# Performance work log

Hardware: AMD Instinct MI355X
Metric: run time of the kernel (lower is better)

The kernel has to match this reference:

```python
import jax, jax.numpy as jnp
import numpy as np

ITERATIONS = 50
EPS = 1.0        # entropy_epsilon
LAM = 1.0
TAU = 1.0 * EPS  # tau = 1 * entropy_epsilon
HALF = 2         # ker_halfsize
SIGMA = 5.0
DN = ('NCHW', 'OIHW', 'NCHW')


def _std_kernel():
    r = jnp.arange(-HALF, HALF + 1, dtype=jnp.float32)
    xx, yy = jnp.meshgrid(r, r, indexing='ij')
    k = jnp.exp(-(xx ** 2 + yy ** 2) / (2.0 * SIGMA ** 2))
    k = k / (k.sum() + 1e-15)
    return k[None, None]  # [1,1,5,5]


_NABLA = jnp.array([[[[0., 0., 0.], [0., -1., 0.], [0., 1., 0.]]],
                    [[[0., 0., 0.], [0., -1., 1.], [0., 0., 0.]]]], dtype=jnp.float32)  # [2,1,3,3]
_DIV = jnp.array([[[[0., -1., 0.], [0., 1., 0.], [0., 0., 0.]],
                   [[0., 0., 0.], [-1., 1., 0.], [0., 0., 0.]]]], dtype=jnp.float32)    # [1,2,3,3]


def _conv(x, w, pad):
    return jax.lax.conv_general_dilated(x, w, (1, 1), [(pad, pad), (pad, pad)],
                                        dimension_numbers=DN)


def setup_inputs() -> dict:
    key = jax.random.key(0)
    o = jax.random.normal(key, (8, 1, 512, 512), dtype=jnp.float32)
    return {"o": o}


def reference(o):
    o = o[:, 0]                      # squeeze channel dim -> [B,H,W]
    B, H, W = o.shape
    ker = _std_kernel()
    # torch.meshgrid(arange(1,H+1), arange(1,W+1)) with 'ij' indexing
    x = jnp.broadcast_to(jnp.arange(1, H + 1, dtype=jnp.float32)[:, None], (H, W))
    y = jnp.broadcast_to(jnp.arange(1, W + 1, dtype=jnp.float32)[None, :], (H, W))

    u0 = jax.nn.sigmoid(o / EPS)
    q0 = jnp.zeros_like(o)

    def step(carry, _):
        u, q, _p, _Tq = carry
        p = _conv(1.0 - 2.0 * u[:, None], ker, HALF)[:, 0]          # [B,H,W]
        s = u.sum((1, 2))                                           # [B]
        cx = (u * x).sum((1, 2)) / s
        cy = (u * y).sum((1, 2)) / s
        dx = x[None] - cx[:, None, None]                            # [B,H,W]
        dy = y[None] - cy[:, None, None]
        cossin = (dx * dy * u).sum((1, 2)) / s
        bsin = (dx ** 2 * u).sum((1, 2)) / s
        asin = (dy ** 2 * u).sum((1, 2)) / s
        Tx = -dx * cossin[:, None, None] + dy * bsin[:, None, None]
        Ty = dy * cossin[:, None, None] - dx * asin[:, None, None]
        Tn = jnp.sqrt(Tx ** 2 + Ty ** 2) + 1e-10
        Tx = Tx / Tn
        Ty = Ty / Tn
        un = _conv(u[:, None], _NABLA, 1)                           # [B,2,H,W]
        q_new = q - TAU * (un[:, 0] * Tx + un[:, 1] * Ty)
        Tq = _conv(jnp.stack([Tx * q_new, Ty * q_new], axis=1), _DIV, 1)[:, 0]
        u_new = jax.nn.sigmoid((o - LAM * p - Tq) / EPS)
        return (u_new, q_new, p, Tq), None

    (u, q, p, Tq), _ = jax.lax.scan(step, (u0, q0, q0, q0), None, length=ITERATIONS)
    u1 = (o - LAM * p - Tq) / EPS
    return u1
```

## Files before the change

### kernel.cpp

```cpp
#include <hip/hip_runtime.h>
#include <math.h>

typedef _Float16 h16;
typedef h16 half8v __attribute__((ext_vector_type(8)));
typedef h16 half4v __attribute__((ext_vector_type(4)));
typedef h16 half2v __attribute__((ext_vector_type(2)));

#define HH 512
#define WW 512
#define BB 8
#define NPIX (HH*WW)
#define NTOT (BB*NPIX)
#define ITER 50

#define TX 64
#define TILE_ROWS 64

#define BLK_PER_BATCH 64
#define PART_ITER_STRIDE (BB*BLK_PER_BATCH*8)

constexpr double W0d = 0.92311634638663587;
constexpr double W1d = 0.98019867330675525;
constexpr double SUM1D = 1.0 + 2.0*(W0d + W1d);
constexpr float  INV_NORM = (float)(1.0/(SUM1D*SUM1D + 1e-15));
constexpr float  W0f = (float)W0d;
constexpr float  W1f = (float)W1d;
constexpr float  S1f = (float)SUM1D;

__device__ __forceinline__ float fast_sigmoid(float x) {
    const float e = __expf(-x);
    return __builtin_amdgcn_rcpf(1.0f + e);
}

__device__ __forceinline__ float edge1d(int v) {
    float r = S1f;
    if (v == 0 || v == HH - 1) r = S1f - W0f - W1f;
    else if (v == 1 || v == HH - 2) r = S1f - W0f;
    return r;
}

union U32H2 { unsigned u; h16 h[2]; };

__device__ __forceinline__ void reduce6_store(float v[6], float* dst8) {
    #pragma unroll
    for (int kk = 0; kk < 6; kk++) {
        float x = v[kk];
        #pragma unroll
        for (int off = 32; off > 0; off >>= 1) x += __shfl_down(x, off, 64);
        v[kk] = x;
    }
    __shared__ float sm[4][6];
    const int lane = threadIdx.x & 63;
    const int wv   = threadIdx.x >> 6;
    if (lane == 0) {
        #pragma unroll
        for (int kk = 0; kk < 6; kk++) sm[wv][kk] = v[kk];
    }
    __syncthreads();
    if (threadIdx.x == 0) {
        float tt[6];
        #pragma unroll
        for (int kk = 0; kk < 6; kk++) tt[kk] = sm[0][kk] + sm[1][kk] + sm[2][kk] + sm[3][kk];
        *(float4*)dst8       = make_float4(tt[0], tt[1], tt[2], tt[3]);
        *(float4*)(dst8 + 4) = make_float4(tt[4], tt[5], 0.f, 0.f);
    }
}

__device__ __forceinline__ void evalF(float uc, float ud, float ur, float qv,
                                      float dx, float dy,
                                      float cossin, float bsin, float asin_,
                                      float& a, float& bv, float& qn) {
    float Tx = -dx * cossin + dy * bsin;
    float Ty =  dy * cossin - dx * asin_;
    const float rn = __builtin_amdgcn_rsqf(Tx * Tx + Ty * Ty + 1e-20f);
    Tx *= rn; Ty *= rn;
    qn = qv - ((ud - uc) * Tx + (ur - uc) * Ty);
    a  = Tx * qn;
    bv = Ty * qn;
}

__global__ __launch_bounds__(256) void init_kernel(const float* __restrict__ o,
                                                   h16* __restrict__ u,
                                                   h16* __restrict__ q,
                                                   h16* __restrict__ oh,
                                                   float* __restrict__ part0) {
    const int b     = blockIdx.x & 7;
    const int chunk = blockIdx.x >> 3;
    const int within = chunk * 4096 + threadIdx.x * 16;
    const int pix = b * NPIX + within;
    const int i = within >> 9;
    const int j = within & (WW - 1);

    float of[16];
    #pragma unroll
    for (int s = 0; s < 4; s++) {
        const float4 ov = *(const float4*)(o + pix + 4 * s);
        of[4*s+0] = ov.x; of[4*s+1] = ov.y; of[4*s+2] = ov.z; of[4*s+3] = ov.w;
    }

    half8v oh8[2], uh8[2], qz8[2];
    float urf[16];
    #pragma unroll
    for (int kk = 0; kk < 16; kk++) {
        oh8[kk >> 3][kk & 7] = (h16)of[kk];
        uh8[kk >> 3][kk & 7] = (h16)fast_sigmoid(of[kk]);
        urf[kk] = (float)uh8[kk >> 3][kk & 7];
        qz8[kk >> 3][kk & 7] = (h16)0.f;
    }
    *(half8v*)(u + pix)      = uh8[0];
    *(half8v*)(u + pix + 8)  = uh8[1];
    *(half8v*)(q + pix)      = qz8[0];
    *(half8v*)(q + pix + 8)  = qz8[1];
    *(half8v*)(oh + pix)     = oh8[0];
    *(half8v*)(oh + pix + 8) = oh8[1];

    const float x = (float)(i + 1);
    float s0 = 0.f, sy = 0.f, syy = 0.f;
    #pragma unroll
    for (int kk = 0; kk < 16; kk++) {
        const float y = (float)(j + 1 + kk);
        s0 += urf[kk]; sy += urf[kk] * y; syy += urf[kk] * y * y;
    }
    float v[6] = {s0, x * s0, sy, x * sy, x * x * s0, syy};
    reduce6_store(v, part0 + ((size_t)b * BLK_PER_BATCH + chunk) * 8);
}

__global__ __launch_bounds__(256) void step_kernel(const h16* __restrict__ oh,
                                                   const h16* __restrict__ uA,
                                                   const h16* __restrict__ qA,
                                                   h16* __restrict__ uB,
                                                   h16* __restrict__ qB,
                                                   const float* __restrict__ partIn,
                                                   float* __restrict__ partOut,
                                                   float* __restrict__ out,
                                                   int lastFlag) {
    const int b    = blockIdx.x & 7;
    const int tile = blockIdx.x >> 3;
    const int j0 = (tile & 7) * TX;
    const int i0 = (tile >> 3) * TILE_ROWS;
    const h16* ubase = uA + (size_t)b * NPIX;
    const h16* qbase = qA + (size_t)b * NPIX;

    const int lin  = threadIdx.x;
    const int lane = lin & 63;
    const int tx = lin & 7;
    const int ty = lin >> 3;
    const int ia = i0 + 2 * ty;
    const int jb = j0 + 8 * tx;
    const int loffA = ia * WW + jb;
    const int loffB = loffA + WW;
    const size_t goffA = (size_t)b * NPIX + loffA;
    const size_t goffB = goffA + WW;

    const bool lok = (jb > 0);
    const bool rok = (jb + 8 < WW);
    const bool ltx = (tx > 0);
    const bool rtx = (tx < 7);

    const float* P0 = partIn + (size_t)b * (BLK_PER_BATCH * 8) + lane * 8;
    const float4 pA0 = *(const float4*)P0;
    const float4 pB0 = *(const float4*)(P0 + 4);

    half8v uM[6];
    unsigned uLbw[6], uRbw[6];
    #pragma unroll
    for (int r = 0; r < 6; r++) {
        const int ii = ia - 2 + r;
        const bool rowok = (ii >= 0 && ii < HH);
        half8v m;
        #pragma unroll
        for (int c = 0; c < 8; c++) m[c] = (h16)0.f;
        unsigned lw = 0u, rw = 0u;
        if (rowok) {
            const h16* rowp = ubase + ii * WW;
            m = *(const half8v*)(rowp + jb);
            if (!ltx && lok) lw = *(const unsigned*)(rowp + jb - 2);
            if (!rtx && rok) rw = *(const unsigned*)(rowp + jb + 8);
        }
        uM[r] = m; uLbw[r] = lw; uRbw[r] = rw;
    }
    const half8v qcA8 = *(const half8v*)(qbase + loffA);
    const half8v qcB8 = *(const half8v*)(qbase + loffB);
    const half8v qu8  = *(const half8v*)(qbase + ((ia > 0) ? loffA - WW : loffA));
    h16 qlA_g = (h16)0.f, qlB_g = (h16)0.f;
    if (!ltx && lok) {
        qlA_g = qbase[loffA - 1];
        qlB_g = qbase[loffB - 1];
    }
    const half8v oA8  = *(const half8v*)(oh + goffA);
    const half8v oB8  = *(const half8v*)(oh + goffB);

    float v6[6] = {pA0.x, pA0.y, pA0.z, pA0.w, pB0.x, pB0.y};
    #pragma unroll
    for (int mask = 1; mask < 64; mask <<= 1) {
        #pragma unroll
        for (int c = 0; c < 6; c++) v6[c] += __shfl_xor(v6[c], mask, 64);
    }
    const double sS  = (double)v6[0];
    const double inv = 1.0 / sS;
    const double cxd = (double)v6[1] * inv;
    const double cyd = (double)v6[2] * inv;
    const float cxf    = (float)cxd;
    const float cyf    = (float)cyd;
    const float cossin = (float)((double)v6[3] * inv - cxd * cyd);
    const float bsin   = (float)((double)v6[4] * inv - cxd * cxd);
    const float asin_  = (float)((double)v6[5] * inv - cyd * cyd);

    unsigned uLw[6], uRw[6];
    #pragma unroll
    for (int r = 0; r < 6; r++) {
        const unsigned w3 = ((const unsigned*)&uM[r])[3];
        const unsigned w0 = ((const unsigned*)&uM[r])[0];
        const unsigned fromL = (unsigned)__shfl((int)w3, lane - 1, 64);
        const unsigned fromR = (unsigned)__shfl((int)w0, lane + 1, 64);
        uLw[r] = ltx ? fromL : uLbw[r];
        uRw[r] = rtx ? fromR : uRbw[r];
    }
    h16 qlAh, qlBh;
    {
        const unsigned qa3 = ((const unsigned*)&qcA8)[3];
        const unsigned qb3 = ((const unsigned*)&qcB8)[3];
        U32H2 ca, cb;
        ca.u = (unsigned)__shfl((int)qa3, lane - 1, 64);
        cb.u = (unsigned)__shfl((int)qb3, lane - 1, 64);
        qlAh = ltx ? ca.h[1] : qlA_g;
        qlBh = ltx ? cb.h[1] : qlB_g;
    }

    float vsA[12], vsB[12];
    float Ue[4][10];
    constexpr float wAr[6] = {W0f, W1f, 1.f, W1f, W0f, 0.f};
    constexpr float wBr[6] = {0.f, W0f, W1f, 1.f, W1f, W0f};
    #pragma unroll
    for (int r = 0; r < 6; r++) {
        float U[12];
        U32H2 cl, cr;
        cl.u = uLw[r]; cr.u = uRw[r];
        U[0] = (float)cl.h[0]; U[1] = (float)cl.h[1];
        #pragma unroll
        for (int c = 0; c < 8; c++) U[c + 2] = (float)uM[r][c];
        U[10] = (float)cr.h[0]; U[11] = (float)cr.h[1];
        #pragma unroll
        for (int c = 0; c < 12; c++) {
            if (r == 0)             vsA[c] = wAr[0] * U[c];
            else if (wAr[r] != 0.f) vsA[c] += wAr[r] * U[c];
            if (r == 1)             vsB[c] = wBr[1] * U[c];
            else if (wBr[r] != 0.f) vsB[c] += wBr[r] * U[c];
        }
        if (r >= 1 && r <= 4) {
            #pragma unroll
            for (int c = 0; c < 10; c++) Ue[r - 1][c] = U[c + 1];
        }
    }

    const float RiA = edge1d(ia);
    const float RiB = edge1d(ia + 1);
    const float dxA = (float)(ia + 1) - cxf;
    const float dxB = (float)(ia + 2) - cxf;
    const float dxu = (float)ia - cxf;

    float blA = 0.f, blB = 0.f;
    {
        const float dyl = (float)jb - cyf;
        float ad, bl, qd;
        evalF(Ue[1][0], Ue[2][0], Ue[1][1], (float)qlAh,
              dxA, dyl, cossin, bsin, asin_, ad, bl, qd);
        if (lok) blA = bl;
        evalF(Ue[2][0], Ue[3][0], Ue[2][1], (float)qlBh,
              dxB, dyl, cossin, bsin, asin_, ad, bl, qd);
        if (lok) blB = bl;
    }

    half8v uhA, uhB, qhA, qhB;
    float s0A = 0.f, syA = 0.f, syyA = 0.f, s0B = 0.f, syB = 0.f, syyB = 0.f;
    float bA_prev = blA, bB_prev = blB;
    #pragma unroll
    for (int k = 0; k < 8; k++) {
        const float Rj = edge1d(jb + k);
        const float cA = W0f * (vsA[k] + vsA[k + 4]) + W1f * (vsA[k + 1] + vsA[k + 3]) + vsA[k + 2];
        const float cB = W0f * (vsB[k] + vsB[k + 4]) + W1f * (vsB[k + 1] + vsB[k + 3]) + vsB[k + 2];
        const float p4A = INV_NORM * (RiA * Rj - 2.0f * cA);
        const float p4B = INV_NORM * (RiB * Rj - 2.0f * cB);

        const float dy = (float)(jb + k + 1) - cyf;
        float aA, bA, qnA;
        evalF(Ue[1][k + 1], Ue[2][k + 1], Ue[1][k + 2], (float)qcA8[k],
              dxA, dy, cossin, bsin, asin_, aA, bA, qnA);
        float au, bu_d, qu_d;
        evalF(Ue[0][k + 1], Ue[1][k + 1], Ue[0][k + 2], (float)qu8[k],
              dxu, dy, cossin, bsin, asin_, au, bu_d, qu_d);
        const float aUA = (ia > 0) ? au : 0.f;
        float aB, bB, qnB;
        evalF(Ue[2][k + 1], Ue[3][k + 1], Ue[2][k + 2], (float)qcB8[k],
              dxB, dy, cossin, bsin, asin_, aB, bB, qnB);

        const float TqA = aA + bA - aUA - bA_prev;
        const float TqB = aB + bB - aA - bB_prev;
        const float tAv = (float)oA8[k] - p4A - TqA;
        const float tBv = (float)oB8[k] - p4B - TqB;

        uhA[k] = (h16)fast_sigmoid(tAv);
        uhB[k] = (h16)fast_sigmoid(tBv);
        qhA[k] = (h16)qnA;
        qhB[k] = (h16)qnB;

        const float urA = (float)uhA[k];
        const float urB = (float)uhB[k];
        const float y = (float)(jb + k + 1);
        s0A += urA; syA += urA * y; syyA += urA * y * y;
        s0B += urB; syB += urB * y; syyB += urB * y * y;

        if (lastFlag) {
            out[goffA + k] = tAv;
            out[goffB + k] = tBv;
        }
        bA_prev = bA; bB_prev = bB;
    }

    *(half8v*)(uB + goffA) = uhA;
    *(half8v*)(uB + goffB) = uhB;
    *(half8v*)(qB + goffA) = qhA;
    *(half8v*)(qB + goffB) = qhB;
    if (lastFlag) return;

    const float xA = (float)(ia + 1);
    const float xB = (float)(ia + 2);
    float v[6] = {s0A + s0B, xA * s0A + xB * s0B, syA + syB,
                  xA * syA + xB * syB, xA * xA * s0A + xB * xB * s0B, syyA + syyB};
    reduce6_store(v, partOut + ((size_t)b * BLK_PER_BATCH + tile) * 8);
}

extern "C" void kernel_launch(void* const* d_in, const int* in_sizes, int n_in,
                              void* d_out, int out_size, void* d_ws, size_t ws_size,
                              hipStream_t stream) {
    const float* o = (const float*)d_in[0];
    float* out = (float*)d_out;

    h16* uA = (h16*)d_ws;
    h16* uB = uA + (size_t)NTOT;
    h16* qA = uB + (size_t)NTOT;
    h16* qB = qA + (size_t)NTOT;
    h16* oh = qB + (size_t)NTOT;
    float* partials = (float*)(oh + (size_t)NTOT);

    init_kernel<<<512, 256, 0, stream>>>(o, uA, qA, oh, partials);

    h16 *ua = uA, *ub = uB, *qa = qA, *qb = qB;
    for (int k = 0; k < ITER; k++) {
        step_kernel<<<512, 256, 0, stream>>>(
            oh, ua, qa, ub, qb,
            partials + (size_t)k * PART_ITER_STRIDE,
            partials + (size_t)(k + 1) * PART_ITER_STRIDE,
            out, (k == ITER - 1) ? 1 : 0);
        h16* tmp;
        tmp = ua; ua = ub; ub = tmp;
        tmp = qa; qa = qb; qb = tmp;
    }
}
```

Measured before the change: 517.4 us.

## Fuse iteration launches into one persistent kernel with per-batch flag barriers

```diff
diff --git a/kernel.cpp b/kernel.cpp
--- a/kernel.cpp
+++ b/kernel.cpp
@@ -3,8 +3,6 @@
 
 typedef _Float16 h16;
 typedef h16 half8v __attribute__((ext_vector_type(8)));
-typedef h16 half4v __attribute__((ext_vector_type(4)));
-typedef h16 half2v __attribute__((ext_vector_type(2)));
 
 #define HH 512
 #define WW 512
@@ -17,7 +15,8 @@
 #define TILE_ROWS 64
 
 #define BLK_PER_BATCH 64
-#define PART_ITER_STRIDE (BB*BLK_PER_BATCH*8)
+#define SLOTF 8
+#define PART_PAR_STRIDE (BB*BLK_PER_BATCH*SLOTF)
 
 constexpr double W0d = 0.92311634638663587;
 constexpr double W1d = 0.98019867330675525;
@@ -27,6 +26,22 @@
 constexpr float  W1f = (float)W1d;
 constexpr float  S1f = (float)SUM1D;
 
+__device__ __forceinline__ unsigned long long ald64(const void* p) {
+    return __hip_atomic_load((unsigned long long*)p, __ATOMIC_RELAXED, __HIP_MEMORY_SCOPE_AGENT);
+}
+__device__ __forceinline__ unsigned ald32(const void* p) {
+    return __hip_atomic_load((unsigned*)p, __ATOMIC_RELAXED, __HIP_MEMORY_SCOPE_AGENT);
+}
+__device__ __forceinline__ void ast64(void* p, unsigned long long v) {
+    __hip_atomic_store((unsigned long long*)p, v, __ATOMIC_RELAXED, __HIP_MEMORY_SCOPE_AGENT);
+}
+__device__ __forceinline__ void ast32(void* p, unsigned v) {
+    __hip_atomic_store((unsigned*)p, v, __ATOMIC_RELAXED, __HIP_MEMORY_SCOPE_AGENT);
+}
+union H8U  { half8v h; unsigned long long u[2]; unsigned w[4]; };
+union U32H2 { unsigned u; h16 h[2]; };
+union U64F2 { unsigned long long u; float f[2]; };
+
 __device__ __forceinline__ float fast_sigmoid(float x) {
     const float e = __expf(-x);
     return __builtin_amdgcn_rcpf(1.0f + e);
@@ -39,9 +54,7 @@
     return r;
 }
 
-union U32H2 { unsigned u; h16 h[2]; };
-
-__device__ __forceinline__ void reduce6_store(float v[6], float* dst8) {
+__device__ __forceinline__ void reduce6_store_tagged(float v[6], float* dst8, float tag) {
     #pragma unroll
     for (int kk = 0; kk < 6; kk++) {
         float x = v[kk];
@@ -61,8 +74,15 @@
         float tt[6];
         #pragma unroll
         for (int kk = 0; kk < 6; kk++) tt[kk] = sm[0][kk] + sm[1][kk] + sm[2][kk] + sm[3][kk];
-        *(float4*)dst8       = make_float4(tt[0], tt[1], tt[2], tt[3]);
-        *(float4*)(dst8 + 4) = make_float4(tt[4], tt[5], 0.f, 0.f);
+        U64F2 w0, w1, w2;
+        w0.f[0] = tt[0]; w0.f[1] = tt[1];
+        w1.f[0] = tt[2]; w1.f[1] = tt[3];
+        w2.f[0] = tt[4]; w2.f[1] = tt[5];
+        ast64(dst8,     w0.u);
+        ast64(dst8 + 2, w1.u);
+        ast64(dst8 + 4, w2.u);
+        asm volatile("s_waitcnt vmcnt(0)" ::: "memory");
+        ast32(dst8 + 7, __float_as_uint(tag));
     }
 }
 
@@ -83,13 +103,18 @@
                                                    h16* __restrict__ u,
                                                    h16* __restrict__ q,
                                                    h16* __restrict__ oh,
-                                                   float* __restrict__ part0) {
+                                                   float* __restrict__ parts) {
     const int b     = blockIdx.x & 7;
     const int chunk = blockIdx.x >> 3;
     const int within = chunk * 4096 + threadIdx.x * 16;
     const int pix = b * NPIX + within;
     const int i = within >> 9;
     const int j = within & (WW - 1);
+
+    if (threadIdx.x == 0) {
+        float* slot0 = parts + ((size_t)b * BLK_PER_BATCH + chunk) * SLOTF;
+        ast32(slot0 + 7, __float_as_uint(0.0f));
+    }
 
     float of[16];
     #pragma unroll
@@ -113,6 +138,7 @@
     *(half8v*)(q + pix + 8)  = qz8[1];
     *(half8v*)(oh + pix)     = oh8[0];
     *(half8v*)(oh + pix + 8) = oh8[1];
+    asm volatile("s_waitcnt vmcnt(0)" ::: "memory");
 
     const float x = (float)(i + 1);
     float s0 = 0.f, sy = 0.f, syy = 0.f;
@@ -122,24 +148,22 @@
         s0 += urf[kk]; sy += urf[kk] * y; syy += urf[kk] * y * y;
     }
     float v[6] = {s0, x * s0, sy, x * sy, x * x * s0, syy};
-    reduce6_store(v, part0 + ((size_t)b * BLK_PER_BATCH + chunk) * 8);
-}
-
-__global__ __launch_bounds__(256) void step_kernel(const h16* __restrict__ oh,
-                                                   const h16* __restrict__ uA,
-                                                   const h16* __restrict__ qA,
-                                                   h16* __restrict__ uB,
-                                                   h16* __restrict__ qB,
-                                                   const float* __restrict__ partIn,
-                                                   float* __restrict__ partOut,
-                                                   float* __restrict__ out,
-                                                   int lastFlag) {
+    float* dst = parts + (size_t)1 * PART_PAR_STRIDE
+                       + ((size_t)b * BLK_PER_BATCH + chunk) * SLOTF;
+    reduce6_store_tagged(v, dst, 1.0f);
+}
+
+__global__ __launch_bounds__(256) void persist_kernel(const h16* __restrict__ ohh,
+                                                      h16* __restrict__ u0,
+                                                      h16* __restrict__ u1,
+                                                      h16* __restrict__ q0,
+                                                      h16* __restrict__ q1,
+                                                      float* __restrict__ parts,
+                                                      float* __restrict__ out) {
     const int b    = blockIdx.x & 7;
     const int tile = blockIdx.x >> 3;
     const int j0 = (tile & 7) * TX;
     const int i0 = (tile >> 3) * TILE_ROWS;
-    const h16* ubase = uA + (size_t)b * NPIX;
-    const h16* qbase = qA + (size_t)b * NPIX;
 
     const int lin  = threadIdx.x;
     const int lane = lin & 63;
@@ -157,177 +181,214 @@
     const bool ltx = (tx > 0);
     const bool rtx = (tx < 7);
 
-    const float* P0 = partIn + (size_t)b * (BLK_PER_BATCH * 8) + lane * 8;
-    const float4 pA0 = *(const float4*)P0;
-    const float4 pB0 = *(const float4*)(P0 + 4);
-
-    half8v uM[6];
-    unsigned uLbw[6], uRbw[6];
-    #pragma unroll
-    for (int r = 0; r < 6; r++) {
-        const int ii = ia - 2 + r;
-        const bool rowok = (ii >= 0 && ii < HH);
-        half8v m;
-        #pragma unroll
-        for (int c = 0; c < 8; c++) m[c] = (h16)0.f;
-        unsigned lw = 0u, rw = 0u;
-        if (rowok) {
-            const h16* rowp = ubase + ii * WW;
-            m = *(const half8v*)(rowp + jb);
-            if (!ltx && lok) lw = *(const unsigned*)(rowp + jb - 2);
-            if (!rtx && rok) rw = *(const unsigned*)(rowp + jb + 8);
-        }
-        uM[r] = m; uLbw[r] = lw; uRbw[r] = rw;
-    }
-    const half8v qcA8 = *(const half8v*)(qbase + loffA);
-    const half8v qcB8 = *(const half8v*)(qbase + loffB);
-    const half8v qu8  = *(const half8v*)(qbase + ((ia > 0) ? loffA - WW : loffA));
-    h16 qlA_g = (h16)0.f, qlB_g = (h16)0.f;
-    if (!ltx && lok) {
-        qlA_g = qbase[loffA - 1];
-        qlB_g = qbase[loffB - 1];
-    }
-    const half8v oA8  = *(const half8v*)(oh + goffA);
-    const half8v oB8  = *(const half8v*)(oh + goffB);
-
-    float v6[6] = {pA0.x, pA0.y, pA0.z, pA0.w, pB0.x, pB0.y};
-    #pragma unroll
-    for (int mask = 1; mask < 64; mask <<= 1) {
-        #pragma unroll
-        for (int c = 0; c < 6; c++) v6[c] += __shfl_xor(v6[c], mask, 64);
-    }
-    const double sS  = (double)v6[0];
-    const double inv = 1.0 / sS;
-    const double cxd = (double)v6[1] * inv;
-    const double cyd = (double)v6[2] * inv;
-    const float cxf    = (float)cxd;
-    const float cyf    = (float)cyd;
-    const float cossin = (float)((double)v6[3] * inv - cxd * cyd);
-    const float bsin   = (float)((double)v6[4] * inv - cxd * cxd);
-    const float asin_  = (float)((double)v6[5] * inv - cyd * cyd);
-
-    unsigned uLw[6], uRw[6];
-    #pragma unroll
-    for (int r = 0; r < 6; r++) {
-        const unsigned w3 = ((const unsigned*)&uM[r])[3];
-        const unsigned w0 = ((const unsigned*)&uM[r])[0];
-        const unsigned fromL = (unsigned)__shfl((int)w3, lane - 1, 64);
-        const unsigned fromR = (unsigned)__shfl((int)w0, lane + 1, 64);
-        uLw[r] = ltx ? fromL : uLbw[r];
-        uRw[r] = rtx ? fromR : uRbw[r];
-    }
-    h16 qlAh, qlBh;
-    {
-        const unsigned qa3 = ((const unsigned*)&qcA8)[3];
-        const unsigned qb3 = ((const unsigned*)&qcB8)[3];
-        U32H2 ca, cb;
-        ca.u = (unsigned)__shfl((int)qa3, lane - 1, 64);
-        cb.u = (unsigned)__shfl((int)qb3, lane - 1, 64);
-        qlAh = ltx ? ca.h[1] : qlA_g;
-        qlBh = ltx ? cb.h[1] : qlB_g;
-    }
-
-    float vsA[12], vsB[12];
-    float Ue[4][10];
-    constexpr float wAr[6] = {W0f, W1f, 1.f, W1f, W0f, 0.f};
-    constexpr float wBr[6] = {0.f, W0f, W1f, 1.f, W1f, W0f};
-    #pragma unroll
-    for (int r = 0; r < 6; r++) {
-        float U[12];
-        U32H2 cl, cr;
-        cl.u = uLw[r]; cr.u = uRw[r];
-        U[0] = (float)cl.h[0]; U[1] = (float)cl.h[1];
-        #pragma unroll
-        for (int c = 0; c < 8; c++) U[c + 2] = (float)uM[r][c];
-        U[10] = (float)cr.h[0]; U[11] = (float)cr.h[1];
-        #pragma unroll
-        for (int c = 0; c < 12; c++) {
-            if (r == 0)             vsA[c] = wAr[0] * U[c];
-            else if (wAr[r] != 0.f) vsA[c] += wAr[r] * U[c];
-            if (r == 1)             vsB[c] = wBr[1] * U[c];
-            else if (wBr[r] != 0.f) vsB[c] += wBr[r] * U[c];
-        }
-        if (r >= 1 && r <= 4) {
-            #pragma unroll
-            for (int c = 0; c < 10; c++) Ue[r - 1][c] = U[c + 1];
-        }
-    }
-
+    const half8v oA8 = *(const half8v*)(ohh + goffA);
+    const half8v oB8 = *(const half8v*)(ohh + goffB);
     const float RiA = edge1d(ia);
     const float RiB = edge1d(ia + 1);
-    const float dxA = (float)(ia + 1) - cxf;
-    const float dxB = (float)(ia + 2) - cxf;
-    const float dxu = (float)ia - cxf;
-
-    float blA = 0.f, blB = 0.f;
-    {
-        const float dyl = (float)jb - cyf;
-        float ad, bl, qd;
-        evalF(Ue[1][0], Ue[2][0], Ue[1][1], (float)qlAh,
-              dxA, dyl, cossin, bsin, asin_, ad, bl, qd);
-        if (lok) blA = bl;
-        evalF(Ue[2][0], Ue[3][0], Ue[2][1], (float)qlBh,
-              dxB, dyl, cossin, bsin, asin_, ad, bl, qd);
-        if (lok) blB = bl;
-    }
-
-    half8v uhA, uhB, qhA, qhB;
-    float s0A = 0.f, syA = 0.f, syyA = 0.f, s0B = 0.f, syB = 0.f, syyB = 0.f;
-    float bA_prev = blA, bB_prev = blB;
-    #pragma unroll
-    for (int k = 0; k < 8; k++) {
-        const float Rj = edge1d(jb + k);
-        const float cA = W0f * (vsA[k] + vsA[k + 4]) + W1f * (vsA[k + 1] + vsA[k + 3]) + vsA[k + 2];
-        const float cB = W0f * (vsB[k] + vsB[k + 4]) + W1f * (vsB[k + 1] + vsB[k + 3]) + vsB[k + 2];
-        const float p4A = INV_NORM * (RiA * Rj - 2.0f * cA);
-        const float p4B = INV_NORM * (RiB * Rj - 2.0f * cB);
-
-        const float dy = (float)(jb + k + 1) - cyf;
-        float aA, bA, qnA;
-        evalF(Ue[1][k + 1], Ue[2][k + 1], Ue[1][k + 2], (float)qcA8[k],
-              dxA, dy, cossin, bsin, asin_, aA, bA, qnA);
-        float au, bu_d, qu_d;
-        evalF(Ue[0][k + 1], Ue[1][k + 1], Ue[0][k + 2], (float)qu8[k],
-              dxu, dy, cossin, bsin, asin_, au, bu_d, qu_d);
-        const float aUA = (ia > 0) ? au : 0.f;
-        float aB, bB, qnB;
-        evalF(Ue[2][k + 1], Ue[3][k + 1], Ue[2][k + 2], (float)qcB8[k],
-              dxB, dy, cossin, bsin, asin_, aB, bB, qnB);
-
-        const float TqA = aA + bA - aUA - bA_prev;
-        const float TqB = aB + bB - aA - bB_prev;
-        const float tAv = (float)oA8[k] - p4A - TqA;
-        const float tBv = (float)oB8[k] - p4B - TqB;
-
-        uhA[k] = (h16)fast_sigmoid(tAv);
-        uhB[k] = (h16)fast_sigmoid(tBv);
-        qhA[k] = (h16)qnA;
-        qhB[k] = (h16)qnB;
-
-        const float urA = (float)uhA[k];
-        const float urB = (float)uhB[k];
-        const float y = (float)(jb + k + 1);
-        s0A += urA; syA += urA * y; syyA += urA * y * y;
-        s0B += urB; syB += urB * y; syyB += urB * y * y;
-
-        if (lastFlag) {
-            out[goffA + k] = tAv;
-            out[goffB + k] = tBv;
-        }
-        bA_prev = bA; bB_prev = bB;
-    }
-
-    *(half8v*)(uB + goffA) = uhA;
-    *(half8v*)(uB + goffB) = uhB;
-    *(half8v*)(qB + goffA) = qhA;
-    *(half8v*)(qB + goffB) = qhB;
-    if (lastFlag) return;
-
     const float xA = (float)(ia + 1);
     const float xB = (float)(ia + 2);
-    float v[6] = {s0A + s0B, xA * s0A + xB * s0B, syA + syB,
-                  xA * syA + xB * syB, xA * xA * s0A + xB * xB * s0B, syyA + syyB};
-    reduce6_store(v, partOut + ((size_t)b * BLK_PER_BATCH + tile) * 8);
+
+    for (int m = 0; m < ITER; m++) {
+        const h16* ua = (m & 1) ? u1 : u0;
+        const h16* qa = (m & 1) ? q1 : q0;
+        h16* ub = (m & 1) ? u0 : u1;
+        h16* qb = (m & 1) ? q0 : q1;
+        const h16* ubase = ua + (size_t)b * NPIX;
+        const h16* qbase = qa + (size_t)b * NPIX;
+
+        const float* slotB = parts + (size_t)((m + 1) & 1) * PART_PAR_STRIDE
+                                   + (size_t)b * BLK_PER_BATCH * SLOTF;
+        const float target = (float)(m + 1);
+        {
+            int guard = 0;
+            for (;;) {
+                const float tg = __uint_as_float(ald32(slotB + lane * SLOTF + 7));
+                if (__all(tg >= target)) break;
+                if (++guard > (1 << 24)) break;
+                __builtin_amdgcn_s_sleep(2);
+            }
+        }
+        asm volatile("" ::: "memory");
+
+        float v6[6];
+        {
+            U64F2 a0, a1, a2;
+            const float* sp = slotB + lane * SLOTF;
+            a0.u = ald64(sp);     a1.u = ald64(sp + 2); a2.u = ald64(sp + 4);
+            v6[0] = a0.f[0]; v6[1] = a0.f[1]; v6[2] = a1.f[0];
+            v6[3] = a1.f[1]; v6[4] = a2.f[0]; v6[5] = a2.f[1];
+        }
+        #pragma unroll
+        for (int mask = 1; mask < 64; mask <<= 1) {
+            #pragma unroll
+            for (int c = 0; c < 6; c++) v6[c] += __shfl_xor(v6[c], mask, 64);
+        }
+        const double sS  = (double)v6[0];
+        const double inv = 1.0 / sS;
+        const double cxd = (double)v6[1] * inv;
+        const double cyd = (double)v6[2] * inv;
+        const float cxf    = (float)cxd;
+        const float cyf    = (float)cyd;
+        const float cossin = (float)((double)v6[3] * inv - cxd * cyd);
+        const float bsin   = (float)((double)v6[4] * inv - cxd * cxd);
+        const float asin_  = (float)((double)v6[5] * inv - cyd * cyd);
+
+        H8U uM[6];
+        unsigned uLbw[6], uRbw[6];
+        #pragma unroll
+        for (int r = 0; r < 6; r++) {
+            const int ii = ia - 2 + r;
+            const bool rowok = (ii >= 0 && ii < HH);
+            H8U mrow; mrow.u[0] = 0ull; mrow.u[1] = 0ull;
+            unsigned lw = 0u, rw = 0u;
+            if (rowok) {
+                const h16* rowp = ubase + ii * WW;
+                mrow.u[0] = ald64(rowp + jb);
+                mrow.u[1] = ald64(rowp + jb + 4);
+                if (!ltx && lok) lw = ald32(rowp + jb - 2);
+                if (!rtx && rok) rw = ald32(rowp + jb + 8);
+            }
+            uM[r] = mrow; uLbw[r] = lw; uRbw[r] = rw;
+        }
+        H8U qcA, qcB, qu;
+        qcA.u[0] = ald64(qbase + loffA); qcA.u[1] = ald64(qbase + loffA + 4);
+        qcB.u[0] = ald64(qbase + loffB); qcB.u[1] = ald64(qbase + loffB + 4);
+        {
+            const int uoff = (ia > 0) ? loffA - WW : loffA;
+            qu.u[0] = ald64(qbase + uoff); qu.u[1] = ald64(qbase + uoff + 4);
+        }
+        h16 qlA_g = (h16)0.f, qlB_g = (h16)0.f;
+        if (!ltx && lok) {
+            U32H2 ta, tb;
+            ta.u = ald32(qbase + loffA - 2);
+            tb.u = ald32(qbase + loffB - 2);
+            qlA_g = ta.h[1]; qlB_g = tb.h[1];
+        }
+
+        unsigned uLw[6], uRw[6];
+        #pragma unroll
+        for (int r = 0; r < 6; r++) {
+            const unsigned w3 = uM[r].w[3];
+            const unsigned w0 = uM[r].w[0];
+            const unsigned fromL = (unsigned)__shfl((int)w3, lane - 1, 64);
+            const unsigned fromR = (unsigned)__shfl((int)w0, lane + 1, 64);
+            uLw[r] = ltx ? fromL : uLbw[r];
+            uRw[r] = rtx ? fromR : uRbw[r];
+        }
+        h16 qlAh, qlBh;
+        {
+            U32H2 ca, cb;
+            ca.u = (unsigned)__shfl((int)qcA.w[3], lane - 1, 64);
+            cb.u = (unsigned)__shfl((int)qcB.w[3], lane - 1, 64);
+            qlAh = ltx ? ca.h[1] : qlA_g;
+            qlBh = ltx ? cb.h[1] : qlB_g;
+        }
+
+        float vsA[12], vsB[12];
+        float Ue[4][10];
+        constexpr float wAr[6] = {W0f, W1f, 1.f, W1f, W0f, 0.f};
+        constexpr float wBr[6] = {0.f, W0f, W1f, 1.f, W1f, W0f};
+        #pragma unroll
+        for (int r = 0; r < 6; r++) {
+            float U[12];
+            U32H2 cl, cr;
+            cl.u = uLw[r]; cr.u = uRw[r];
+            U[0] = (float)cl.h[0]; U[1] = (float)cl.h[1];
+            #pragma unroll
+            for (int c = 0; c < 8; c++) U[c + 2] = (float)uM[r].h[c];
+            U[10] = (float)cr.h[0]; U[11] = (float)cr.h[1];
+            #pragma unroll
+            for (int c = 0; c < 12; c++) {
+                if (r == 0)             vsA[c] = wAr[0] * U[c];
+                else if (wAr[r] != 0.f) vsA[c] += wAr[r] * U[c];
+                if (r == 1)             vsB[c] = wBr[1] * U[c];
+                else if (wBr[r] != 0.f) vsB[c] += wBr[r] * U[c];
+            }
+            if (r >= 1 && r <= 4) {
+                #pragma unroll
+                for (int c = 0; c < 10; c++) Ue[r - 1][c] = U[c + 1];
+            }
+        }
+
+        const float dxA = xA - cxf;
+        const float dxB = xB - cxf;
+        const float dxu = (float)ia - cxf;
+
+        float blA = 0.f, blB = 0.f;
+        {
+            const float dyl = (float)jb - cyf;
+            float ad, bl, qd;
+            evalF(Ue[1][0], Ue[2][0], Ue[1][1], (float)qlAh,
+                  dxA, dyl, cossin, bsin, asin_, ad, bl, qd);
+            if (lok) blA = bl;
+            evalF(Ue[2][0], Ue[3][0], Ue[2][1], (float)qlBh,
+                  dxB, dyl, cossin, bsin, asin_, ad, bl, qd);
+            if (lok) blB = bl;
+        }
+
+        half8v uhA, uhB, qhA, qhB;
+        float s0A = 0.f, syA = 0.f, syyA = 0.f, s0B = 0.f, syB = 0.f, syyB = 0.f;
+        float bA_prev = blA, bB_prev = blB;
+        #pragma unroll
+        for (int k = 0; k < 8; k++) {
+            const float Rj = edge1d(jb + k);
+            const float cA = W0f * (vsA[k] + vsA[k + 4]) + W1f * (vsA[k + 1] + vsA[k + 3]) + vsA[k + 2];
+            const float cB = W0f * (vsB[k] + vsB[k + 4]) + W1f * (vsB[k + 1] + vsB[k + 3]) + vsB[k + 2];
+            const float p4A = INV_NORM * (RiA * Rj - 2.0f * cA);
+            const float p4B = INV_NORM * (RiB * Rj - 2.0f * cB);
+
+            const float dy = (float)(jb + k + 1) - cyf;
+            float aA, bA, qnA;
+            evalF(Ue[1][k + 1], Ue[2][k + 1], Ue[1][k + 2], (float)qcA.h[k],
+                  dxA, dy, cossin, bsin, asin_, aA, bA, qnA);
+            float au, bu_d, qu_d;
+            evalF(Ue[0][k + 1], Ue[1][k + 1], Ue[0][k + 2], (float)qu.h[k],
+                  dxu, dy, cossin, bsin, asin_, au, bu_d, qu_d);
+            const float aUA = (ia > 0) ? au : 0.f;
+            float aB, bB, qnB;
+            evalF(Ue[2][k + 1], Ue[3][k + 1], Ue[2][k + 2], (float)qcB.h[k],
+                  dxB, dy, cossin, bsin, asin_, aB, bB, qnB);
+
+            const float TqA = aA + bA - aUA - bA_prev;
+            const float TqB = aB + bB - aA - bB_prev;
+            const float tAv = (float)oA8[k] - p4A - TqA;
+            const float tBv = (float)oB8[k] - p4B - TqB;
+
+            uhA[k] = (h16)fast_sigmoid(tAv);
+            uhB[k] = (h16)fast_sigmoid(tBv);
+            qhA[k] = (h16)qnA;
+            qhB[k] = (h16)qnB;
+
+            const float urA = (float)uhA[k];
+            const float urB = (float)uhB[k];
+            const float y = (float)(jb + k + 1);
+            s0A += urA; syA += urA * y; syyA += urA * y * y;
+            s0B += urB; syB += urB * y; syyB += urB * y * y;
+
+            if (m == ITER - 1) {
+                out[goffA + k] = tAv;
+                out[goffB + k] = tBv;
+            }
+            bA_prev = bA; bB_prev = bB;
+        }
+
+        if (m == ITER - 1) return;
+
+        {
+            H8U su, sq;
+            su.h = uhA; ast64(ub + goffA, su.u[0]); ast64(ub + goffA + 4, su.u[1]);
+            su.h = uhB; ast64(ub + goffB, su.u[0]); ast64(ub + goffB + 4, su.u[1]);
+            sq.h = qhA; ast64(qb + goffA, sq.u[0]); ast64(qb + goffA + 4, sq.u[1]);
+            sq.h = qhB; ast64(qb + goffB, sq.u[0]); ast64(qb + goffB + 4, sq.u[1]);
+        }
+        asm volatile("s_waitcnt vmcnt(0)" ::: "memory");
+
+        float v[6] = {s0A + s0B, xA * s0A + xB * s0B, syA + syB,
+                      xA * syA + xB * syB, xA * xA * s0A + xB * xB * s0B, syyA + syyB};
+        float* dst = parts + (size_t)(m & 1) * PART_PAR_STRIDE
+                           + ((size_t)b * BLK_PER_BATCH + tile) * SLOTF;
+        reduce6_store_tagged(v, dst, (float)(m + 2));
+    }
 }
 
 extern "C" void kernel_launch(void* const* d_in, const int* in_sizes, int n_in,
@@ -336,24 +397,14 @@
     const float* o = (const float*)d_in[0];
     float* out = (float*)d_out;
 
-    h16* uA = (h16*)d_ws;
-    h16* uB = uA + (size_t)NTOT;
-    h16* qA = uB + (size_t)NTOT;
-    h16* qB = qA + (size_t)NTOT;
-    h16* oh = qB + (size_t)NTOT;
-    float* partials = (float*)(oh + (size_t)NTOT);
-
-    init_kernel<<<512, 256, 0, stream>>>(o, uA, qA, oh, partials);
-
-    h16 *ua = uA, *ub = uB, *qa = qA, *qb = qB;
-    for (int k = 0; k < ITER; k++) {
-        step_kernel<<<512, 256, 0, stream>>>(
-            oh, ua, qa, ub, qb,
-            partials + (size_t)k * PART_ITER_STRIDE,
-            partials + (size_t)(k + 1) * PART_ITER_STRIDE,
-            out, (k == ITER - 1) ? 1 : 0);
-        h16* tmp;
-        tmp = ua; ua = ub; ub = tmp;
-        tmp = qa; qa = qb; qb = tmp;
-    }
-}
+    h16* u0 = (h16*)d_ws;
+    h16* u1 = u0 + (size_t)NTOT;
+    h16* q0 = u1 + (size_t)NTOT;
+    h16* q1 = q0 + (size_t)NTOT;
+    h16* oh = q1 + (size_t)NTOT;
+    float* parts = (float*)(oh + (size_t)NTOT);
+
+    init_kernel<<<512, 256, 0, stream>>>(o, u0, q0, oh, parts);
+
+    persist_kernel<<<512, 256, 0, stream>>>(oh, u0, u1, q0, q1, parts, out);
+}
```

Result: slower. 961.0 us (+85.7%).
